# Performance work log

Hardware: AMD Instinct MI355X
Metric: run time of the kernel (lower is better)

The kernel has to match this reference:

```python
import jax, jax.numpy as jnp
import numpy as np
import math

E = 1024   # embedding_size
H = 16     # layer_size (num heads)
DK = 64    # key_size
DH = 64    # head_size
HID = 4096 # hidden_size
B = 2
S = 2048   # context_size
EPS = 1e-5


def layer_norm(x, w, b):
    mu = jnp.mean(x, axis=-1, keepdims=True)
    var = jnp.mean(jnp.square(x - mu), axis=-1, keepdims=True)
    return (x - mu) * jax.lax.rsqrt(var + EPS) * w + b


def setup_inputs() -> dict:
    key = jax.random.key(0)
    ks = jax.random.split(key, 16)
    sE = 1.0 / math.sqrt(E)
    sH = 1.0 / math.sqrt(HID)
    return {
        "embeddings": jax.random.normal(ks[0], (B, S, E), dtype=jnp.float32),
        "Wq": jax.random.uniform(ks[1], (H, E, DK), minval=-sE, maxval=sE, dtype=jnp.float32),
        "bq": jnp.zeros((H, DK), dtype=jnp.float32),
        "Wk": jax.random.uniform(ks[2], (H, E, DK), minval=-sE, maxval=sE, dtype=jnp.float32),
        "bk": jnp.zeros((H, DK), dtype=jnp.float32),
        "Wv": jax.random.uniform(ks[3], (H, E, DH), minval=-sE, maxval=sE, dtype=jnp.float32),
        "bv": jnp.zeros((H, DH), dtype=jnp.float32),
        "ln1_w": jnp.ones((E,), dtype=jnp.float32),
        "ln1_b": jnp.zeros((E,), dtype=jnp.float32),
        "ln2_w": jnp.ones((E,), dtype=jnp.float32),
        "ln2_b": jnp.zeros((E,), dtype=jnp.float32),
        "W1": jax.random.uniform(ks[4], (E, HID), minval=-sE, maxval=sE, dtype=jnp.float32),
        "b1": jnp.zeros((HID,), dtype=jnp.float32),
        "W2": jax.random.uniform(ks[5], (HID, E), minval=-sH, maxval=sH, dtype=jnp.float32),
        "b2": jnp.zeros((E,), dtype=jnp.float32),
    }


def reference(embeddings, Wq, bq, Wk, bk, Wv, bv, ln1_w, ln1_b, ln2_w, ln2_b, W1, b1, W2, b2):
    # NOTE: faithful to source: residual uses the POST-norm activations
    # (embeddings is reassigned to the LayerNorm output before the residual add).
    x = layer_norm(embeddings, ln1_w, ln1_b)            # [B,S,E]
    q = jnp.einsum('bse,hed->bhsd', x, Wq) + bq[:, None, :]
    k = jnp.einsum('bse,hed->bhsd', x, Wk) + bk[:, None, :]
    v = jnp.einsum('bse,hed->bhsd', x, Wv) + bv[:, None, :]
    scores = jnp.einsum('bhsd,bhtd->bhst', q, k) / math.sqrt(DK)  # [B,H,S,S]
    causal = jnp.tril(jnp.ones((S, S), dtype=bool))
    scores = jnp.where(causal, scores, -jnp.inf)
    w = jax.nn.softmax(scores, axis=-1)
    o = jnp.einsum('bhst,bhtd->bhsd', w, v)             # [B,H,S,DH]
    o = jnp.transpose(o, (0, 2, 1, 3)).reshape(B, S, H * DH)  # concat heads
    x = x + o
    y = layer_norm(x, ln2_w, ln2_b)
    h = jax.nn.relu(jnp.einsum('bse,eh->bsh', y, W1) + b1)
    out = y + jnp.einsum('bsh,he->bse', h, W2) + b2
    return out
```

## Files before the change

### kernel.cpp

```cpp
#include <hip/hip_runtime.h>


typedef unsigned short u16;
typedef unsigned int   u32;
typedef __bf16 bf16x8 __attribute__((ext_vector_type(8)));
typedef float  f32x4  __attribute__((ext_vector_type(4)));

#define NEG_INF (-__builtin_inff())

#if __has_builtin(__builtin_amdgcn_exp2f)
#define EXP2F(x) __builtin_amdgcn_exp2f(x)
#else
#define EXP2F(x) exp2f(x)
#endif

__device__ __forceinline__ u32 pack_bf16_trunc(float a, float b) {
#if __has_builtin(__builtin_amdgcn_perm)
  return __builtin_amdgcn_perm(__float_as_uint(b), __float_as_uint(a), 0x07060302u);
#else
  return (__float_as_uint(a) >> 16) | (__float_as_uint(b) & 0xFFFF0000u);
#endif
}

__device__ __forceinline__ u16 f2b(float f) {
  u32 u = __float_as_uint(f);
  u = (u + 0x7fffu + ((u >> 16) & 1u)) >> 16;
  return (u16)u;
}

__device__ __forceinline__ void gload16(const void* g, void* l) {
  __builtin_amdgcn_global_load_lds(
      (const __attribute__((address_space(1))) u32*)g,
      (__attribute__((address_space(3))) u32*)l, 16, 0, 0);
}

__device__ __forceinline__ bf16x8 ld16(const u16* p) { return *(const bf16x8*)p; }

__global__ __launch_bounds__(256)
void transpose_all_k(const float* __restrict__ W1, const float* __restrict__ W2,
                     const float* __restrict__ Wq, const float* __restrict__ Wk,
                     const float* __restrict__ Wv,
                     u16* __restrict__ W1t, u16* __restrict__ W2t,
                     u16* __restrict__ Wqkv_t) {
  __shared__ float tile[64][65];
  int id = blockIdx.x;
  const float* in; u16* out; int R, C, r0, c0;
  if (id < 1024) {
    in = W1; out = W1t; R = 1024; C = 4096;
    r0 = (id & 15) * 64; c0 = (id >> 4) * 64;
  } else if (id < 2048) {
    id -= 1024;
    in = W2; out = W2t; R = 4096; C = 1024;
    r0 = (id >> 4) * 64; c0 = (id & 15) * 64;
  } else {
    id -= 2048;
    int z = id >> 4, which = z >> 4, sub = z & 15;
    const float* base = which == 0 ? Wq : (which == 1 ? Wk : Wv);
    in = base + (size_t)sub * 1024 * 64;
    out = Wqkv_t + (size_t)which * 1024 * 1024 + (size_t)sub * 64 * 1024;
    R = 1024; C = 64;
    r0 = (id & 15) * 64; c0 = 0;
  }
  int tr = threadIdx.x >> 6, tc = threadIdx.x & 63;
#pragma unroll
  for (int i = 0; i < 16; i++) {
    int r = i * 4 + tr;
    tile[r][tc] = in[(size_t)(r0 + r) * C + c0 + tc];
  }
  __syncthreads();
#pragma unroll
  for (int i = 0; i < 16; i++) {
    int c = i * 4 + tr;
    out[(size_t)(c0 + c) * R + r0 + tc] = f2b(tile[tc][c]);
  }
}

__global__ __launch_bounds__(256)
void vtrans_k(const u16* __restrict__ vin, u16* __restrict__ vt) {
  __shared__ __align__(16) u16 tile[64][72];
  int s0 = blockIdx.x * 64, bh = blockIdx.y;
  const u16* ip = vin + (size_t)bh * 2048 * 64;
  u16* op = vt + (size_t)bh * 64 * 2048;
  int t = threadIdx.x;
#pragma unroll
  for (int i = 0; i < 2; i++) {
    int idx = i * 256 + t, r = idx >> 3, c = idx & 7;
    *(uint4*)&tile[r][c * 8] = *(const uint4*)(ip + (size_t)(s0 + r) * 64 + c * 8);
  }
  __syncthreads();
#pragma unroll
  for (int i = 0; i < 16; i++) {
    int d = i * 4 + (t >> 6), s = t & 63;
    op[(size_t)d * 2048 + s0 + s] = tile[s][d];
  }
}

__global__ __launch_bounds__(256)
void ln_k(const float* __restrict__ in, const float* __restrict__ in2,
          const float* __restrict__ w, const float* __restrict__ b,
          float* __restrict__ outf, u16* __restrict__ outb) {
  int row = blockIdx.x, t = threadIdx.x;
  const float4* ip = (const float4*)(in + (size_t)row * 1024);
  float4 x = ip[t];
  if (in2) {
    const float4* ip2 = (const float4*)(in2 + (size_t)row * 1024);
    float4 o = ip2[t];
    x.x += o.x; x.y += o.y; x.z += o.z; x.w += o.w;
  }
  float s = x.x + x.y + x.z + x.w;
  float q = x.x * x.x + x.y * x.y + x.z * x.z + x.w * x.w;
#pragma unroll
  for (int m = 32; m; m >>= 1) { s += __shfl_xor(s, m); q += __shfl_xor(q, m); }
  __shared__ float rs[4], rq[4];
  if ((t & 63) == 0) { rs[t >> 6] = s; rq[t >> 6] = q; }
  __syncthreads();
  s = rs[0] + rs[1] + rs[2] + rs[3];
  q = rq[0] + rq[1] + rq[2] + rq[3];
  float mean = s * (1.f / 1024.f);
  float var  = q * (1.f / 1024.f) - mean * mean;
  float rstd = rsqrtf(var + 1e-5f);
  float4 wv = ((const float4*)w)[t];
  float4 bv = ((const float4*)b)[t];
  float4 y;
  y.x = (x.x - mean) * rstd * wv.x + bv.x;
  y.y = (x.y - mean) * rstd * wv.y + bv.y;
  y.z = (x.z - mean) * rstd * wv.z + bv.z;
  y.w = (x.w - mean) * rstd * wv.w + bv.w;
  if (outf) ((float4*)(outf + (size_t)row * 1024))[t] = y;
  ushort4 ub;
  ub.x = f2b(y.x); ub.y = f2b(y.y); ub.z = f2b(y.z); ub.w = f2b(y.w);
  ((ushort4*)(outb + (size_t)row * 1024))[t] = ub;
}

#define EPI_QKV  0
#define EPI_RELU 1
#define EPI_RES  2

#define QSCALE 0.18033688011112042f

template <int EPI>
__device__ __forceinline__
void gemm_body(const u16* __restrict__ A, const u16* __restrict__ Bt,
               int K, int lda, int ldbt,
               const float* __restrict__ bias0, const float* __restrict__ bias1,
               const float* __restrict__ bias2, const float* __restrict__ res,
               int ldout, u16* __restrict__ outb, float* __restrict__ outf,
               float* __restrict__ outp) {
  __shared__ __align__(16) u16 As[2][128 * 64];
  __shared__ __align__(16) u16 Bs[2][128 * 64];
  int t = threadIdx.x;
  int wave = t >> 6, lane = t & 63, quad = lane >> 4, l16 = lane & 15;
  int x7 = l16 & 7;
  int wm = (wave >> 1) * 64, wn = (wave & 1) * 64;
  int bm = blockIdx.x * 128, bn = blockIdx.y * 128;
  int zoff = blockIdx.z * K;

  const u16* Agl[4];
  const u16* Bgl[4];
#pragma unroll
  for (int i = 0; i < 4; i++) {
    int idx = i * 256 + t, r = idx >> 3, c = (idx & 7) ^ (r & 7);
    Agl[i] = A + (size_t)(bm + r) * lda + zoff + c * 8;
    Bgl[i] = Bt + (size_t)(bn + r) * ldbt + zoff + c * 8;
  }

  f32x4 acc[4][4] = {};

#pragma unroll
  for (int i = 0; i < 4; i++) {
    gload16(Agl[i], (u16*)As[0] + t * 8 + i * 2048);
    gload16(Bgl[i], (u16*)Bs[0] + t * 8 + i * 2048);
  }
  __syncthreads();

  int nk = K >> 6;
  for (int kt = 0; kt < nk; kt++) {
    const u16* Ac = As[kt & 1];
    const u16* Bc = Bs[kt & 1];
    if (kt + 1 < nk) {
      int k1 = (kt + 1) << 6;
      u16* An = (u16*)As[(kt + 1) & 1] + t * 8;
      u16* Bn = (u16*)Bs[(kt + 1) & 1] + t * 8;
#pragma unroll
      for (int i = 0; i < 4; i++) {
        gload16(Agl[i] + k1, An + i * 2048);
        gload16(Bgl[i] + k1, Bn + i * 2048);
      }
    }
#pragma unroll
    for (int kc = 0; kc < 2; kc++) {
      bf16x8 af[4], bfr[4];
#pragma unroll
      for (int i = 0; i < 4; i++) {
        int r = wm + i * 16 + l16;
        af[i] = *(const bf16x8*)(Ac + r * 64 + (((kc * 4 + quad) ^ x7) * 8));
      }
#pragma unroll
      for (int j = 0; j < 4; j++) {
        int r = wn + j * 16 + l16;
        bfr[j] = *(const bf16x8*)(Bc + r * 64 + (((kc * 4 + quad) ^ x7) * 8));
      }
#pragma unroll
      for (int i = 0; i < 4; i++)
#pragma unroll
        for (int j = 0; j < 4; j++)
          acc[i][j] = __builtin_amdgcn_mfma_f32_16x16x32_bf16(af[i], bfr[j],
                                                              acc[i][j], 0, 0, 0);
    }
    __syncthreads();
  }

#pragma unroll
  for (int i = 0; i < 4; i++) {
#pragma unroll
    for (int j = 0; j < 4; j++) {
      int c = bn + wn + j * 16 + l16;
#pragma unroll
      for (int rr = 0; rr < 4; rr++) {
        int r = bm + wm + i * 16 + quad * 4 + rr;
        float v = acc[i][j][rr];
        if (EPI == EPI_QKV) {
          int which = c >> 10, h = (c >> 6) & 15, d = c & 63;
          const float* bp = which == 0 ? bias0 : (which == 1 ? bias1 : bias2);
          v += bp[h * 64 + d];
          if (which == 0) v *= QSCALE;
          int bb = r >> 11, ss = r & 2047;
          outb[((size_t)(which * 32 + bb * 16 + h) * 2048 + ss) * 64 + d] = f2b(v);
        } else if (EPI == EPI_RELU) {
          v += bias0[c];
          v = v > 0.f ? v : 0.f;
          outb[(size_t)r * ldout + c] = f2b(v);
        } else {
          if (blockIdx.z == 0) {
            v += bias0[c] + res[(size_t)r * ldout + c];
            outf[(size_t)r * ldout + c] = v;
          } else {
            outp[(size_t)r * ldout + c] = v;
          }
        }
      }
    }
  }
}

__global__ __launch_bounds__(256)
void qkv_gemm(const u16* A, const u16* Bt, int K, int lda, int ldbt,
              const float* b0, const float* b1, const float* b2,
              u16* outb) {
  gemm_body<EPI_QKV>(A, Bt, K, lda, ldbt, b0, b1, b2, nullptr, 0, outb, nullptr, nullptr);
}
__global__ __launch_bounds__(256)
void ffn1_gemm(const u16* A, const u16* Bt, int K, int lda, int ldbt,
               const float* b0, int ldout, u16* outb) {
  gemm_body<EPI_RELU>(A, Bt, K, lda, ldbt, b0, nullptr, nullptr, nullptr, ldout, outb, nullptr, nullptr);
}
__global__ __launch_bounds__(256)
void ffn2_gemm(const u16* A, const u16* Bt, int K, int lda, int ldbt,
               const float* b0, const float* res, int ldout,
               float* outf, float* outp) {
  gemm_body<EPI_RES>(A, Bt, K, lda, ldbt, b0, nullptr, nullptr, res, ldout, nullptr, outf, outp);
}

__global__ __launch_bounds__(256)
void reduce_k(float* __restrict__ out, const float* __restrict__ part) {
  int i = blockIdx.x * 256 + threadIdx.x;
  float4 a = ((const float4*)part)[i];
  float4 b = ((float4*)out)[i];
  b.x += a.x; b.y += a.y; b.z += a.z; b.w += a.w;
  ((float4*)out)[i] = b;
}

__global__ __launch_bounds__(512, 6)
void attn_k(const u16* __restrict__ qkv, const u16* __restrict__ vt,
            float* __restrict__ o) {
  int bh = blockIdx.y, b = bh >> 4, h = bh & 15;
  int Qt = b ? (15 - (int)blockIdx.x) : (int)blockIdx.x;
  int t = threadIdx.x;
  int wave = t >> 6, lane = t & 63, quad = lane >> 4, l16 = lane & 15;
  int x7 = l16 & 7;
  int q0 = Qt * 128 + wave * 16;

  const u16* qg = qkv + (size_t)bh * (2048 * 64);
  const u16* kg = qkv + (size_t)(32 + bh) * (2048 * 64);
  const u16* vg = vt + (size_t)bh * (64 * 2048);

  __shared__ __align__(16) u16 Ks[2][64 * 64];
  __shared__ __align__(16) u16 Vs[2][64 * 64];
  __shared__ __align__(16) u16 Ps[8][16 * 64 + 32];
  u16* Pw = Ps[wave];
  float* auxf = (float*)(Pw + 1024);

  int sr = t >> 3, sc_ = (t & 7) ^ (sr & 7);

  gload16(kg + (size_t)sr * 64 + sc_ * 8, Ks[0] + t * 8);
  gload16(vg + (size_t)sr * 2048 + sc_ * 8, Vs[0] + t * 8);

  bf16x8 qf0 = ld16(qg + (size_t)(q0 + l16) * 64 + quad * 8);
  bf16x8 qf1 = ld16(qg + (size_t)(q0 + l16) * 64 + 32 + quad * 8);

  f32x4 oacc[4] = {};
  float mo = NEG_INF, ll = 0.f;
  int kmax_w = q0 >> 6;
  int klast = 2 * Qt + 1;

  __syncthreads();

  for (int kt = 0; kt <= klast; kt++) {
    const u16* ks = Ks[kt & 1];
    const u16* vs = Vs[kt & 1];
    if (kt < klast) {
      gload16(kg + (size_t)((kt + 1) * 64 + sr) * 64 + sc_ * 8, Ks[(kt + 1) & 1] + t * 8);
      gload16(vg + (size_t)sr * 2048 + (kt + 1) * 64 + sc_ * 8, Vs[(kt + 1) & 1] + t * 8);
    }
    if (kt <= kmax_w) {
      f32x4 sc[4];
#pragma unroll
      for (int g = 0; g < 4; g++) {
        const u16* kr = ks + (g * 16 + l16) * 64;
        bf16x8 kf0 = *(const bf16x8*)(kr + ((quad ^ x7) * 8));
        bf16x8 kf1 = *(const bf16x8*)(kr + (((4 + quad) ^ x7) * 8));
        f32x4 s = {};
        s = __builtin_amdgcn_mfma_f32_16x16x32_bf16(kf0, qf0, s, 0, 0, 0);
        s = __builtin_amdgcn_mfma_f32_16x16x32_bf16(kf1, qf1, s, 0, 0, 0);
        sc[g] = s;
      }

      if (kt == kmax_w) {
#pragma unroll
        for (int g = 0; g < 4; g++) {
          int kvb = kt * 64 + g * 16 + quad * 4;
#pragma unroll
          for (int rr = 0; rr < 4; rr++)
            if (kvb + rr > q0 + l16) sc[g][rr] = NEG_INF;
        }
      }

      float mx = sc[0][0];
#pragma unroll
      for (int g = 0; g < 4; g++)
#pragma unroll
        for (int rr = 0; rr < 4; rr++) mx = fmaxf(mx, sc[g][rr]);
      mx = fmaxf(mx, __shfl_xor(mx, 16));
      mx = fmaxf(mx, __shfl_xor(mx, 32));
      float mnew = fmaxf(mo, mx);
      float al = EXP2F(mo - mnew);
      mo = mnew;

      float sum = 0.f;
#pragma unroll
      for (int g = 0; g < 4; g++) {
        float p0 = EXP2F(sc[g][0] - mnew);
        float p1 = EXP2F(sc[g][1] - mnew);
        float p2 = EXP2F(sc[g][2] - mnew);
        float p3 = EXP2F(sc[g][3] - mnew);
        sum += (p0 + p1) + (p2 + p3);
        u32 lo = pack_bf16_trunc(p0, p1);
        u32 hi = pack_bf16_trunc(p2, p3);
        int slot = (2 * g + (quad >> 1)) ^ x7;
        *(uint2*)(Pw + l16 * 64 + slot * 8 + (quad & 1) * 4) = make_uint2(lo, hi);
      }
      sum += __shfl_xor(sum, 16);
      sum += __shfl_xor(sum, 32);
      ll = ll * al + sum;

      if (lane < 16) auxf[lane] = al;
      f32x4 av = *(const f32x4*)(auxf + quad * 4);
#pragma unroll
      for (int g = 0; g < 4; g++)
#pragma unroll
        for (int rr = 0; rr < 4; rr++) oacc[g][rr] *= av[rr];

      bf16x8 pf0 = *(const bf16x8*)(Pw + l16 * 64 + ((quad ^ x7) * 8));
      bf16x8 pf1 = *(const bf16x8*)(Pw + l16 * 64 + (((4 + quad) ^ x7) * 8));
#pragma unroll
      for (int g = 0; g < 4; g++) {
        const u16* vr = vs + (g * 16 + l16) * 64;
        bf16x8 vf0 = *(const bf16x8*)(vr + ((quad ^ x7) * 8));
        bf16x8 vf1 = *(const bf16x8*)(vr + (((4 + quad) ^ x7) * 8));
        oacc[g] = __builtin_amdgcn_mfma_f32_16x16x32_bf16(pf0, vf0, oacc[g], 0, 0, 0);
        oacc[g] = __builtin_amdgcn_mfma_f32_16x16x32_bf16(pf1, vf1, oacc[g], 0, 0, 0);
      }
    }
    __syncthreads();
  }

  if (lane < 16) auxf[lane] = ll;
  f32x4 lv = *(const f32x4*)(auxf + quad * 4);
  float rinv[4];
#pragma unroll
  for (int rr = 0; rr < 4; rr++) rinv[rr] = 1.f / lv[rr];
  float* op = o + ((size_t)b * 2048 + q0) * 1024 + h * 64;
#pragma unroll
  for (int g = 0; g < 4; g++)
#pragma unroll
    for (int rr = 0; rr < 4; rr++)
      op[(size_t)(quad * 4 + rr) * 1024 + g * 16 + l16] = oacc[g][rr] * rinv[rr];
}

extern "C" void kernel_launch(void* const* d_in, const int* in_sizes, int n_in,
                              void* d_out, int out_size, void* d_ws, size_t ws_size,
                              hipStream_t stream) {
  const float* emb  = (const float*)d_in[0];
  const float* Wq   = (const float*)d_in[1];
  const float* bq   = (const float*)d_in[2];
  const float* Wk   = (const float*)d_in[3];
  const float* bk   = (const float*)d_in[4];
  const float* Wv   = (const float*)d_in[5];
  const float* bv   = (const float*)d_in[6];
  const float* ln1w = (const float*)d_in[7];
  const float* ln1b = (const float*)d_in[8];
  const float* ln2w = (const float*)d_in[9];
  const float* ln2b = (const float*)d_in[10];
  const float* W1   = (const float*)d_in[11];
  const float* b1   = (const float*)d_in[12];
  const float* W2   = (const float*)d_in[13];
  const float* b2   = (const float*)d_in[14];
  float* out = (float*)d_out;

  char* p = (char*)d_ws;
  u16*   Wqkv_t = (u16*)p;   p += (size_t)3072 * 1024 * 2;
  u16*   W1t    = (u16*)p;   p += (size_t)4096 * 1024 * 2;
  u16*   W2t    = (u16*)p;   p += (size_t)1024 * 4096 * 2;
  float* x      = (float*)p; p += (size_t)4096 * 1024 * 4;
  u16*   xb     = (u16*)p;   p += (size_t)4096 * 1024 * 2;
  u16*   qkvb   = (u16*)p;   p += (size_t)3 * 32 * 2048 * 64 * 2;
  float* ob     = (float*)p; p += (size_t)4096 * 1024 * 4;
  float* y      = (float*)p; p += (size_t)4096 * 1024 * 4;
  u16*   yb     = (u16*)p;   p += (size_t)4096 * 1024 * 2;
  u16*   hb     = (u16*)qkvb;
  u16*   vT     = (u16*)y;
  float* part   = x;
  if (ws_size < (size_t)(p - (char*)d_ws)) return;

  transpose_all_k<<<dim3(2816), 256, 0, stream>>>(
      W1, W2, Wq, Wk, Wv, W1t, W2t, Wqkv_t);

  ln_k<<<dim3(4096), 256, 0, stream>>>(emb, nullptr, ln1w, ln1b, x, xb);

  qkv_gemm<<<dim3(32, 24, 1), 256, 0, stream>>>(
      xb, Wqkv_t, 1024, 1024, 1024, bq, bk, bv, qkvb);

  vtrans_k<<<dim3(32, 32), 256, 0, stream>>>(qkvb + (size_t)64 * 2048 * 64, vT);

  attn_k<<<dim3(16, 32), 512, 0, stream>>>(qkvb, vT, ob);

  ln_k<<<dim3(4096), 256, 0, stream>>>(x, ob, ln2w, ln2b, y, yb);

  ffn1_gemm<<<dim3(32, 32, 1), 256, 0, stream>>>(
      yb, W1t, 1024, 1024, 1024, b1, 4096, hb);

  ffn2_gemm<<<dim3(32, 8, 2), 256, 0, stream>>>(
      hb, W2t, 2048, 4096, 4096, b2, y, 1024, out, part);

  reduce_k<<<dim3(4096), 256, 0, stream>>>(out, part);
}
```

Measured before the change: 328.2 us.

## Use larger 256-row tiles with 512-thread blocks for FFN GEMMs

```diff
diff --git a/kernel.cpp b/kernel.cpp
--- a/kernel.cpp
+++ b/kernel.cpp
@@ -138,14 +138,11 @@
 
 #define QSCALE 0.18033688011112042f
 
-template <int EPI>
 __device__ __forceinline__
-void gemm_body(const u16* __restrict__ A, const u16* __restrict__ Bt,
-               int K, int lda, int ldbt,
-               const float* __restrict__ bias0, const float* __restrict__ bias1,
-               const float* __restrict__ bias2, const float* __restrict__ res,
-               int ldout, u16* __restrict__ outb, float* __restrict__ outf,
-               float* __restrict__ outp) {
+void gemm_qkv_body(const u16* __restrict__ A, const u16* __restrict__ Bt,
+                   int K, int lda, int ldbt,
+                   const float* __restrict__ bias0, const float* __restrict__ bias1,
+                   const float* __restrict__ bias2, u16* __restrict__ outb) {
   __shared__ __align__(16) u16 As[2][128 * 64];
   __shared__ __align__(16) u16 Bs[2][128 * 64];
   int t = threadIdx.x;
@@ -153,15 +150,14 @@
   int x7 = l16 & 7;
   int wm = (wave >> 1) * 64, wn = (wave & 1) * 64;
   int bm = blockIdx.x * 128, bn = blockIdx.y * 128;
-  int zoff = blockIdx.z * K;
 
   const u16* Agl[4];
   const u16* Bgl[4];
 #pragma unroll
   for (int i = 0; i < 4; i++) {
     int idx = i * 256 + t, r = idx >> 3, c = (idx & 7) ^ (r & 7);
-    Agl[i] = A + (size_t)(bm + r) * lda + zoff + c * 8;
-    Bgl[i] = Bt + (size_t)(bn + r) * ldbt + zoff + c * 8;
+    Agl[i] = A + (size_t)(bm + r) * lda + c * 8;
+    Bgl[i] = Bt + (size_t)(bn + r) * ldbt + c * 8;
   }
 
   f32x4 acc[4][4] = {};
@@ -219,14 +215,111 @@
       for (int rr = 0; rr < 4; rr++) {
         int r = bm + wm + i * 16 + quad * 4 + rr;
         float v = acc[i][j][rr];
-        if (EPI == EPI_QKV) {
-          int which = c >> 10, h = (c >> 6) & 15, d = c & 63;
-          const float* bp = which == 0 ? bias0 : (which == 1 ? bias1 : bias2);
-          v += bp[h * 64 + d];
-          if (which == 0) v *= QSCALE;
-          int bb = r >> 11, ss = r & 2047;
-          outb[((size_t)(which * 32 + bb * 16 + h) * 2048 + ss) * 64 + d] = f2b(v);
-        } else if (EPI == EPI_RELU) {
+        int which = c >> 10, h = (c >> 6) & 15, d = c & 63;
+        const float* bp = which == 0 ? bias0 : (which == 1 ? bias1 : bias2);
+        v += bp[h * 64 + d];
+        if (which == 0) v *= QSCALE;
+        int bb = r >> 11, ss = r & 2047;
+        outb[((size_t)(which * 32 + bb * 16 + h) * 2048 + ss) * 64 + d] = f2b(v);
+      }
+    }
+  }
+}
+
+__global__ __launch_bounds__(256)
+void qkv_gemm(const u16* A, const u16* Bt, int K, int lda, int ldbt,
+              const float* b0, const float* b1, const float* b2,
+              u16* outb) {
+  gemm_qkv_body(A, Bt, K, lda, ldbt, b0, b1, b2, outb);
+}
+
+template <int EPI, int BN>
+__device__ __forceinline__
+void gemm256_body(const u16* __restrict__ A, const u16* __restrict__ Bt,
+                  int K, int lda, int ldbt,
+                  const float* __restrict__ bias0, const float* __restrict__ res,
+                  int ldout, u16* __restrict__ outb, float* __restrict__ outf,
+                  float* __restrict__ outp) {
+  constexpr int NW = BN / 64;
+  constexpr int MW = 8 / NW;
+  constexpr int MR = (256 / MW) / 16;
+  __shared__ __align__(16) u16 As[2][256 * 64];
+  __shared__ __align__(16) u16 Bs[2][BN * 64];
+  int t = threadIdx.x;
+  int wave = t >> 6, lane = t & 63, quad = lane >> 4, l16 = lane & 15;
+  int x7 = l16 & 7;
+  int wr0 = (wave / NW) * (256 / MW);
+  int wc0 = (wave % NW) * 64;
+  int bm = blockIdx.x * 256, bn = blockIdx.y * BN;
+  int zoff = blockIdx.z * K;
+
+  const u16* Ag[4];
+  const u16* Bg[NW];
+#pragma unroll
+  for (int i = 0; i < 4; i++) {
+    int idx = i * 512 + t, r = idx >> 3, c = (idx & 7) ^ (r & 7);
+    Ag[i] = A + (size_t)(bm + r) * lda + zoff + c * 8;
+  }
+#pragma unroll
+  for (int i = 0; i < NW; i++) {
+    int idx = i * 512 + t, r = idx >> 3, c = (idx & 7) ^ (r & 7);
+    Bg[i] = Bt + (size_t)(bn + r) * ldbt + zoff + c * 8;
+  }
+
+  f32x4 acc[MR][4] = {};
+
+#pragma unroll
+  for (int i = 0; i < 4; i++) gload16(Ag[i], (u16*)As[0] + t * 8 + i * 4096);
+#pragma unroll
+  for (int i = 0; i < NW; i++) gload16(Bg[i], (u16*)Bs[0] + t * 8 + i * 4096);
+  __syncthreads();
+
+  int nk = K >> 6;
+  for (int kt = 0; kt < nk; kt++) {
+    const u16* Ac = As[kt & 1];
+    const u16* Bc = Bs[kt & 1];
+    if (kt + 1 < nk) {
+      int k1 = (kt + 1) << 6;
+      u16* An = (u16*)As[(kt + 1) & 1] + t * 8;
+      u16* Bn = (u16*)Bs[(kt + 1) & 1] + t * 8;
+#pragma unroll
+      for (int i = 0; i < 4; i++) gload16(Ag[i] + k1, An + i * 4096);
+#pragma unroll
+      for (int i = 0; i < NW; i++) gload16(Bg[i] + k1, Bn + i * 4096);
+    }
+#pragma unroll
+    for (int kc = 0; kc < 2; kc++) {
+      bf16x8 af[MR], bfr[4];
+#pragma unroll
+      for (int i = 0; i < MR; i++) {
+        int r = wr0 + i * 16 + l16;
+        af[i] = *(const bf16x8*)(Ac + r * 64 + (((kc * 4 + quad) ^ x7) * 8));
+      }
+#pragma unroll
+      for (int j = 0; j < 4; j++) {
+        int r = wc0 + j * 16 + l16;
+        bfr[j] = *(const bf16x8*)(Bc + r * 64 + (((kc * 4 + quad) ^ x7) * 8));
+      }
+#pragma unroll
+      for (int i = 0; i < MR; i++)
+#pragma unroll
+        for (int j = 0; j < 4; j++)
+          acc[i][j] = __builtin_amdgcn_mfma_f32_16x16x32_bf16(af[i], bfr[j],
+                                                              acc[i][j], 0, 0, 0);
+    }
+    __syncthreads();
+  }
+
+#pragma unroll
+  for (int i = 0; i < MR; i++) {
+#pragma unroll
+    for (int j = 0; j < 4; j++) {
+      int c = bn + wc0 + j * 16 + l16;
+#pragma unroll
+      for (int rr = 0; rr < 4; rr++) {
+        int r = bm + wr0 + i * 16 + quad * 4 + rr;
+        float v = acc[i][j][rr];
+        if (EPI == EPI_RELU) {
           v += bias0[c];
           v = v > 0.f ? v : 0.f;
           outb[(size_t)r * ldout + c] = f2b(v);
@@ -243,22 +336,19 @@
   }
 }
 
-__global__ __launch_bounds__(256)
-void qkv_gemm(const u16* A, const u16* Bt, int K, int lda, int ldbt,
-              const float* b0, const float* b1, const float* b2,
-              u16* outb) {
-  gemm_body<EPI_QKV>(A, Bt, K, lda, ldbt, b0, b1, b2, nullptr, 0, outb, nullptr, nullptr);
-}
-__global__ __launch_bounds__(256)
+__global__ __launch_bounds__(512, 2)
 void ffn1_gemm(const u16* A, const u16* Bt, int K, int lda, int ldbt,
                const float* b0, int ldout, u16* outb) {
-  gemm_body<EPI_RELU>(A, Bt, K, lda, ldbt, b0, nullptr, nullptr, nullptr, ldout, outb, nullptr, nullptr);
-}
-__global__ __launch_bounds__(256)
+  gemm256_body<EPI_RELU, 256>(A, Bt, K, lda, ldbt, b0, nullptr, ldout, outb,
+                              nullptr, nullptr);
+}
+
+__global__ __launch_bounds__(512, 2)
 void ffn2_gemm(const u16* A, const u16* Bt, int K, int lda, int ldbt,
                const float* b0, const float* res, int ldout,
                float* outf, float* outp) {
-  gemm_body<EPI_RES>(A, Bt, K, lda, ldbt, b0, nullptr, nullptr, res, ldout, nullptr, outf, outp);
+  gemm256_body<EPI_RES, 128>(A, Bt, K, lda, ldbt, b0, res, ldout,
+                             nullptr, outf, outp);
 }
 
 __global__ __launch_bounds__(256)
@@ -446,10 +536,10 @@
 
   ln_k<<<dim3(4096), 256, 0, stream>>>(x, ob, ln2w, ln2b, y, yb);
 
-  ffn1_gemm<<<dim3(32, 32, 1), 256, 0, stream>>>(
+  ffn1_gemm<<<dim3(16, 16, 1), 512, 0, stream>>>(
       yb, W1t, 1024, 1024, 1024, b1, 4096, hb);
 
-  ffn2_gemm<<<dim3(32, 8, 2), 256, 0, stream>>>(
+  ffn2_gemm<<<dim3(16, 8, 2), 512, 0, stream>>>(
       hb, W2t, 2048, 4096, 4096, b2, y, 1024, out, part);
 
   reduce_k<<<dim3(4096), 256, 0, stream>>>(out, part);
```

After: 333.9 us. About the same (+1.7%).
